# Kernel tuning notes

Hardware: AMD Instinct MI355X
Metric: run time of the kernel (lower is better)

## Reference

```python
import jax, jax.numpy as jnp
import numpy as np
from jax.scipy.linalg import solve_triangular

REG = 1e-6  # reg_covar added to covariance diagonal
LOG2PI = float(np.log(2.0 * np.pi))
RESP_EPS = 10.0 * float(np.finfo(np.float32).eps)


def _log_gauss(X, means, covs):
    # X: [N,D], means: [K,D], covs: [K,D,D] -> per-sample per-component log N(x|mu_k, Sigma_k): [N,K]
    K, D = means.shape
    eye = jnp.eye(D, dtype=X.dtype)
    chol = jnp.linalg.cholesky(covs + REG * eye)                      # [K,D,D]
    diff = X[None, :, :] - means[:, None, :]                          # [K,N,D]
    sol = jax.vmap(lambda L, d: solve_triangular(L, d.T, lower=True))(chol, diff)  # [K,D,N]
    maha = jnp.sum(sol * sol, axis=1)                                 # [K,N]
    logdet = jnp.sum(jnp.log(jnp.diagonal(chol, axis1=1, axis2=2)), axis=1)  # [K] = 0.5*log|Sigma|
    return (-0.5 * (D * LOG2PI + maha) - logdet[:, None]).T           # [N,K]


def _em_step(X, weights, means, covs):
    N, D = X.shape
    # E-step: responsibilities via stable logsumexp
    lp = _log_gauss(X, means, covs) + jnp.log(weights)[None, :]       # [N,K]
    log_norm = jax.scipy.special.logsumexp(lp, axis=1)                # [N]
    resp = jnp.exp(lp - log_norm[:, None])                            # [N,K]
    # M-step (MLE)
    nk = resp.sum(axis=0) + RESP_EPS                                  # [K]
    new_w = nk / N
    new_means = (resp.T @ X) / nk[:, None]                            # [K,D]
    diff = X[None, :, :] - new_means[:, None, :]                      # [K,N,D]
    new_covs = jnp.einsum('kn,knd,kne->kde', resp.T, diff, diff) / nk[:, None, None]
    new_covs = new_covs + REG * jnp.eye(D, dtype=X.dtype)
    return new_w, new_means, new_covs


def reference(X, weights, means, covariances, n_iter):
    # Normalize provided weights (uniform init in the torch module)
    w0 = weights / jnp.sum(weights)

    def step(carry, _):
        w, m, c = carry
        return _em_step(X, w, m, c), None

    (w, m, c), _ = jax.lax.scan(step, (w0, means, covariances), xs=None, length=n_iter)
    # Final per-sample log-likelihood under the fitted mixture (lower bound)
    lp = _log_gauss(X, m, c) + jnp.log(w)[None, :]
    return jax.scipy.special.logsumexp(lp, axis=1)                    # [N]


def setup_inputs() -> dict:
    key = jax.random.key(0)
    kx, km = jax.random.split(key)
    N, D, K = 100000, 32, 16
    X = jax.random.normal(kx, (N, D), dtype=jnp.float32)
    weights = jnp.ones((K,), dtype=jnp.float32) / K
    means = jax.random.normal(km, (K, D), dtype=jnp.float32)
    covariances = jnp.tile(jnp.eye(D, dtype=jnp.float32)[None], (K, 1, 1))
    return {"X": X, "weights": weights, "means": means, "covariances": covariances, "n_iter": 5}
```

## Files before the change

kernel.cpp:

```cpp
#include <hip/hip_runtime.h>
#include <math.h>

#define REGC 1e-6f
#define LOG2PI 1.83787706640934534f
#define RESP_EPS 1.1920929e-6f

#define PART_K 1156
#define RS 16

typedef __attribute__((ext_vector_type(8))) short short8;
typedef __attribute__((ext_vector_type(4))) float f32x4;
typedef unsigned short ushort_t;
typedef unsigned int uint_t;

__device__ __forceinline__ ushort_t f2bf(float x) {
    uint_t u = __float_as_uint(x);
    uint_t r = (u + 0x7fffu + ((u >> 16) & 1u)) >> 16;
    return (ushort_t)r;
}
__device__ __forceinline__ float bf2f(ushort_t h) {
    return __uint_as_float(((uint_t)h) << 16);
}
__device__ __forceinline__ f32x4 shx4(f32x4 v, int m) {
    f32x4 r;
#pragma unroll
    for (int i = 0; i < 4; ++i) r[i] = __shfl_xor(v[i], m);
    return r;
}
__device__ __forceinline__ f32x4 sel4(bool s, f32x4 b, f32x4 a) {
    f32x4 r;
#pragma unroll
    for (int i = 0; i < 4; ++i) r[i] = s ? b[i] : a[i];
    return r;
}
__device__ __forceinline__ short8 pack_rx(const float* r8, const short8 bh, float& row) {
    uint_t u[8];
#pragma unroll
    for (int jj = 0; jj < 8; ++jj) {
        float av = r8[jj] * bf2f((ushort_t)bh[jj]);
        row += av;
        u[jj] = __float_as_uint(av) + 0x8000u;
    }
    short8 out;
    uint_t* o = (uint_t*)&out;
    o[0] = __builtin_amdgcn_perm(u[1], u[0], 0x07060302);
    o[1] = __builtin_amdgcn_perm(u[3], u[2], 0x07060302);
    o[2] = __builtin_amdgcn_perm(u[5], u[4], 0x07060302);
    o[3] = __builtin_amdgcn_perm(u[7], u[6], 0x07060302);
    return out;
}

__global__ __launch_bounds__(256) void gmm_xsplit(const float* __restrict__ X,
                                                  ushort_t* __restrict__ Xh,
                                                  ushort_t* __restrict__ Xl,
                                                  ushort_t* __restrict__ XTH,
                                                  int N) {
    int chunk = blockIdx.x;
    int t = threadIdx.x;
    __shared__ float xsh[32][33];
    int s = t >> 3, q = t & 7;
    int n = chunk * 32 + s;
    float4 v = make_float4(0.f, 0.f, 0.f, 0.f);
    if (n < N) v = ((const float4*)(X + (size_t)n * 32))[q];
    float vv[4] = { v.x, v.y, v.z, v.w };
    xsh[s][q * 4 + 0] = v.x; xsh[s][q * 4 + 1] = v.y;
    xsh[s][q * 4 + 2] = v.z; xsh[s][q * 4 + 3] = v.w;
    if (n < N) {
        ushort_t h[4], l[4];
#pragma unroll
        for (int i = 0; i < 4; ++i) {
            h[i] = f2bf(vv[i]);
            l[i] = f2bf(vv[i] - bf2f(h[i]));
        }
        size_t o = (size_t)n * 32 + q * 4;
        *(uint2*)(Xh + o) = make_uint2((uint_t)h[0] | ((uint_t)h[1] << 16),
                                       (uint_t)h[2] | ((uint_t)h[3] << 16));
        *(uint2*)(Xl + o) = make_uint2((uint_t)l[0] | ((uint_t)l[1] << 16),
                                       (uint_t)l[2] | ((uint_t)l[3] << 16));
    }
    __syncthreads();
    int di = t >> 7;
    int lane = (t >> 1) & 63;
    int jj0 = (t & 1) * 4;
    int c = lane & 15, quad = lane >> 4;
    int d = di * 16 + c;
    ushort_t fh[4];
#pragma unroll
    for (int i = 0; i < 4; ++i) fh[i] = f2bf(xsh[quad * 8 + jj0 + i][d]);
    size_t fo = ((size_t)(chunk * 2 + di) * 64 + lane) * 8 + jj0;
    *(uint2*)(XTH + fo) = make_uint2((uint_t)fh[0] | ((uint_t)fh[1] << 16),
                                     (uint_t)fh[2] | ((uint_t)fh[3] << 16));
}

__global__ __launch_bounds__(64) void gmm_prep0(const float* __restrict__ w,
                                                const float* __restrict__ mu,
                                                const float* __restrict__ cov,
                                                ushort_t* __restrict__ Wh,
                                                ushort_t* __restrict__ Wl,
                                                float* __restrict__ Bv,
                                                float* __restrict__ Cc) {
    int k = blockIdx.x;
    int t = threadIdx.x;
    __shared__ float L[32][33];
    __shared__ float Ai[32][33];
    const float* cv = cov + (size_t)k * 1024;
    const float* muk = mu + (size_t)k * 32;
#pragma unroll
    for (int rep = 0; rep < 16; ++rep) {
        int idx = rep * 64 + t;
        int i = idx >> 5, j = idx & 31;
        L[i][j] = cv[idx] + (i == j ? REGC : 0.f);
    }
    __syncthreads();
#pragma unroll
    for (int j = 0; j < 32; ++j) {
        float s = L[j][j];
#pragma unroll
        for (int p = 0; p < j; ++p) { float v = L[j][p]; s -= v * v; }
        float dj = sqrtf(s);
        if (t > j && t < 32) {
            float s2 = L[t][j];
#pragma unroll
            for (int p = 0; p < j; ++p) s2 -= L[t][p] * L[j][p];
            L[t][j] = s2 / dj;
        }
        if (t == j) L[j][j] = dj;
        __syncthreads();
    }
    if (t < 32) {
        float ai[32];
#pragma unroll
        for (int r = 0; r < 32; ++r) {
            float s = (r == t) ? 1.f : 0.f;
#pragma unroll
            for (int p = 0; p < r; ++p) s -= L[r][p] * ai[p];
            ai[r] = s / L[r][r];
        }
#pragma unroll
        for (int r = 0; r < 32; ++r) Ai[r][t] = ai[r];
    }
    __syncthreads();
#pragma unroll
    for (int rep = 0; rep < 16; ++rep) {
        int idx = rep * 64 + t;
        int i = idx >> 5, j = idx & 31;
        float v = Ai[i][j];
        ushort_t h = f2bf(v);
        Wh[(size_t)(k * 32 + i) * 32 + j] = h;
        Wl[(size_t)(k * 32 + i) * 32 + j] = f2bf(v - bf2f(h));
    }
    if (t < 32) {
        float s = 0.f;
#pragma unroll
        for (int j = 0; j < 32; ++j) s += Ai[t][j] * muk[j];
        Bv[k * 32 + t] = s;
    }
    float wsum = 0.f;
#pragma unroll
    for (int i = 0; i < 16; ++i) wsum += w[i];
    float lv = (t < 32) ? logf(L[t & 31][t & 31]) : 0.f;
#pragma unroll
    for (int off = 1; off < 32; off <<= 1) lv += __shfl_xor(lv, off);
    if (t == 0) Cc[k] = logf(w[k] / wsum) - 0.5f * 32.0f * LOG2PI - lv;
}

__global__ __launch_bounds__(1024) __attribute__((amdgpu_waves_per_eu(4, 4)))
void gmm_emstep(const ushort_t* __restrict__ Xh, const ushort_t* __restrict__ Xl,
                const ushort_t* __restrict__ XTH,
                const ushort_t* __restrict__ Wh, const ushort_t* __restrict__ Wl,
                const float* __restrict__ Bv, const float* __restrict__ Cc,
                float* __restrict__ part, int N) {
    __shared__ float rsh[16][516];
    int t = threadIdx.x;
    int wave = t >> 6, lane = t & 63;
    int quad = lane >> 4, c = lane & 15;

    int wstart0 = (int)blockIdx.x * 512 + wave * 32;
    bool dup = (wstart0 + 32 > N);
    int wst = dup ? ((N >= 32) ? N - 32 : 0) : wstart0;

    size_t xo0 = (size_t)(wst + c) * 32 + quad * 8;
    size_t xo1 = (size_t)(wst + 16 + c) * 32 + quad * 8;
    short8 ah0 = *(const short8*)(Xh + xo0);
    short8 al0 = *(const short8*)(Xl + xo0);
    short8 ah1 = *(const short8*)(Xh + xo1);
    short8 al1 = *(const short8*)(Xl + xo1);

    {
        f32x4 p0[2], p1[2], p2[2], p3[2], fin[2];
#pragma unroll
        for (int k = 0; k < 16; ++k) {
            size_t w0 = (size_t)(k * 32 + c) * 32 + quad * 8;
            size_t w1 = w0 + 512;
            short8 bh0 = *(const short8*)(Wh + w0);
            short8 bl0 = *(const short8*)(Wl + w0);
            short8 bh1 = *(const short8*)(Wh + w1);
            short8 bl1 = *(const short8*)(Wl + w1);
            float bv0 = Bv[k * 32 + c];
            float bv1 = Bv[k * 32 + 16 + c];
#pragma unroll
            for (int tt = 0; tt < 2; ++tt) {
                short8 ah = tt ? ah1 : ah0;
                short8 al = tt ? al1 : al0;
                f32x4 a0 = {0.f, 0.f, 0.f, 0.f};
                f32x4 a1 = {0.f, 0.f, 0.f, 0.f};
                a0 = __builtin_amdgcn_mfma_f32_16x16x32_bf16(ah, bh0, a0, 0, 0, 0);
                a0 = __builtin_amdgcn_mfma_f32_16x16x32_bf16(ah, bl0, a0, 0, 0, 0);
                a0 = __builtin_amdgcn_mfma_f32_16x16x32_bf16(al, bh0, a0, 0, 0, 0);
                a1 = __builtin_amdgcn_mfma_f32_16x16x32_bf16(ah, bh1, a1, 0, 0, 0);
                a1 = __builtin_amdgcn_mfma_f32_16x16x32_bf16(ah, bl1, a1, 0, 0, 0);
                a1 = __builtin_amdgcn_mfma_f32_16x16x32_bf16(al, bh1, a1, 0, 0, 0);
                f32x4 ms;
#pragma unroll
                for (int r = 0; r < 4; ++r) {
                    float d0 = a0[r] - bv0;
                    float d1 = a1[r] - bv1;
                    ms[r] = fmaf(d0, d0, d1 * d1);
                }
                if ((k & 1) == 0) { p0[tt] = ms; }
                else {
                    f32x4 a = p0[tt] + shx4(p0[tt], 1);
                    f32x4 b = ms + shx4(ms, 1);
                    f32x4 v = sel4((c & 1) != 0, b, a);
                    if ((k & 2) == 0) { p1[tt] = v; }
                    else {
                        a = p1[tt] + shx4(p1[tt], 2); b = v + shx4(v, 2); v = sel4((c & 2) != 0, b, a);
                        if ((k & 4) == 0) { p2[tt] = v; }
                        else {
                            a = p2[tt] + shx4(p2[tt], 4); b = v + shx4(v, 4); v = sel4((c & 4) != 0, b, a);
                            if ((k & 8) == 0) { p3[tt] = v; }
                            else {
                                a = p3[tt] + shx4(p3[tt], 8); b = v + shx4(v, 8);
                                fin[tt] = sel4((c & 8) != 0, b, a);
                            }
                        }
                    }
                }
            }
        }
        float ccv = Cc[c];
#pragma unroll
        for (int tt = 0; tt < 2; ++tt) {
            f32x4 lp;
#pragma unroll
            for (int r = 0; r < 4; ++r) lp[r] = ccv - 0.5f * fin[tt][r];
            f32x4 mx = lp;
#pragma unroll
            for (int off = 1; off < 16; off <<= 1) {
                f32x4 s = shx4(mx, off);
#pragma unroll
                for (int r = 0; r < 4; ++r) mx[r] = fmaxf(mx[r], s[r]);
            }
            f32x4 e;
#pragma unroll
            for (int r = 0; r < 4; ++r) e[r] = __expf(lp[r] - mx[r]);
            f32x4 sm = e;
#pragma unroll
            for (int off = 1; off < 16; off <<= 1) sm = sm + shx4(sm, off);
            f32x4 sv;
#pragma unroll
            for (int r = 0; r < 4; ++r) sv[r] = dup ? 0.f : e[r] / sm[r];
            *(f32x4*)&rsh[c][wave * 32 + tt * 16 + quad * 4] = sv;
        }
    }
    __syncthreads();

    {
        int k = wave;
        f32x4 m00 = {0.f,0.f,0.f,0.f}, m01 = {0.f,0.f,0.f,0.f};
        f32x4 m10 = {0.f,0.f,0.f,0.f}, m11 = {0.f,0.f,0.f,0.f};
        float row0 = 0.f, row1 = 0.f, corner = 0.f;
#pragma unroll 4
        for (int ch = 0; ch < 16; ++ch) {
            size_t fb = (((size_t)((int)blockIdx.x * 16 + ch)) * 128 + lane) * 8;
            short8 bh0 = *(const short8*)(XTH + fb);
            short8 bh1 = *(const short8*)(XTH + fb + 512);
            float r8[8];
#pragma unroll
            for (int jj = 0; jj < 8; ++jj) r8[jj] = rsh[k][ch * 32 + quad * 8 + jj];
            corner += ((r8[0]+r8[1])+(r8[2]+r8[3])) + ((r8[4]+r8[5])+(r8[6]+r8[7]));
            short8 a0 = pack_rx(r8, bh0, row0);
            short8 a1 = pack_rx(r8, bh1, row1);
            m00 = __builtin_amdgcn_mfma_f32_16x16x32_bf16(a0, bh0, m00, 0, 0, 0);
            m01 = __builtin_amdgcn_mfma_f32_16x16x32_bf16(a0, bh1, m01, 0, 0, 0);
            m10 = __builtin_amdgcn_mfma_f32_16x16x32_bf16(a1, bh0, m10, 0, 0, 0);
            m11 = __builtin_amdgcn_mfma_f32_16x16x32_bf16(a1, bh1, m11, 0, 0, 0);
        }
        row0 += __shfl_xor(row0, 16);  row0 += __shfl_xor(row0, 32);
        row1 += __shfl_xor(row1, 16);  row1 += __shfl_xor(row1, 32);
        corner += __shfl_xor(corner, 16);  corner += __shfl_xor(corner, 32);

        float* pb = part + ((size_t)blockIdx.x * 16 + k) * PART_K;
#pragma unroll
        for (int r = 0; r < 4; ++r) {
            pb[(quad * 4 + r) * 34 + c]           = m00[r];
            pb[(quad * 4 + r) * 34 + 16 + c]      = m01[r];
            pb[(16 + quad * 4 + r) * 34 + c]      = m10[r];
            pb[(16 + quad * 4 + r) * 34 + 16 + c] = m11[r];
        }
        if (quad == 0) {
            pb[32 * 34 + c]      = row0;
            pb[32 * 34 + 16 + c] = row1;
        }
        if (lane == 0) pb[32 * 34 + 32] = corner;
    }
}

__global__ __launch_bounds__(256) void gmm_reduce1(const float* __restrict__ part,
                                                   float* __restrict__ part2,
                                                   int npart) {
    int k = blockIdx.x, g = blockIdx.y;
    int nb = (npart + RS - 1) / RS;
    int b0 = g * nb;
    int b1 = b0 + nb; if (b1 > npart) b1 = npart;
    for (int idx = threadIdx.x; idx < PART_K; idx += 256) {
        float s = 0.f;
#pragma unroll 4
        for (int b = b0; b < b1; ++b)
            s += part[((size_t)b * 16 + k) * PART_K + idx];
        part2[((size_t)g * 16 + k) * PART_K + idx] = s;
    }
}

__global__ __launch_bounds__(1024) void gmm_redfin_prep(const float* __restrict__ part2,
                                                        ushort_t* __restrict__ Wh,
                                                        ushort_t* __restrict__ Wl,
                                                        float* __restrict__ Bv,
                                                        float* __restrict__ Cc,
                                                        int N) {
    int k = blockIdx.x;
    int t = threadIdx.x;
    __shared__ float S[1156];
    __shared__ float L[1056];
    __shared__ float Ai[1056];
    __shared__ float mean[32];

    for (int idx = t; idx < 1121; idx += 1024) {
        float s = 0.f;
#pragma unroll
        for (int b = 0; b < RS; ++b)
            s += part2[((size_t)b * 16 + k) * PART_K + idx];
        S[idx] = s;
    }
    __syncthreads();
    float nk = S[32 * 34 + 32] + RESP_EPS;
    float inv = 1.f / nk;
    {
        int i = t >> 5, j = t & 31;
        float mi = S[32 * 34 + i] * inv;
        float mj = S[32 * 34 + j] * inv;
        L[i * 33 + j] = S[i * 34 + j] * inv - mi * mj + ((i == j) ? 2.f * REGC : 0.f);
    }
    if (t < 32) mean[t] = S[32 * 34 + t] * inv;
    __syncthreads();

#pragma unroll
    for (int j = 0; j < 32; ++j) {
        if (t < 32) {
            float s = L[j * 33 + j];
#pragma unroll
            for (int p = 0; p < j; ++p) { float v = L[j * 33 + p]; s -= v * v; }
            float dj = sqrtf(s);
            if (t > j) {
                float s2 = L[t * 33 + j];
#pragma unroll
                for (int p = 0; p < j; ++p) s2 -= L[t * 33 + p] * L[j * 33 + p];
                L[t * 33 + j] = s2 / dj;
            }
            if (t == j) L[j * 33 + j] = dj;
        }
        __syncthreads();
    }
    if (t < 32) {
        float ai[32];
#pragma unroll
        for (int r = 0; r < 32; ++r) {
            float s = (r == t) ? 1.f : 0.f;
#pragma unroll
            for (int p = 0; p < r; ++p) s -= L[r * 33 + p] * ai[p];
            ai[r] = s / L[r * 33 + r];
        }
#pragma unroll
        for (int r = 0; r < 32; ++r) Ai[r * 33 + t] = ai[r];
    }
    __syncthreads();
    {
        int i = t >> 5, j = t & 31;
        float v = Ai[i * 33 + j];
        ushort_t h = f2bf(v);
        Wh[(size_t)(k * 32 + i) * 32 + j] = h;
        Wl[(size_t)(k * 32 + i) * 32 + j] = f2bf(v - bf2f(h));
    }
    if (t < 32) {
        float s = 0.f;
#pragma unroll
        for (int j = 0; j < 32; ++j) s += Ai[t * 33 + j] * mean[j];
        Bv[k * 32 + t] = s;
    }
    float lv = (t < 32) ? logf(L[(t & 31) * 33 + (t & 31)]) : 0.f;
#pragma unroll
    for (int off = 1; off < 32; off <<= 1) lv += __shfl_xor(lv, off);
    if (t == 0) Cc[k] = logf(nk / (float)N) - 0.5f * 32.0f * LOG2PI - lv;
}

__global__ __launch_bounds__(256, 2) void gmm_estep_fin(const ushort_t* __restrict__ Xh,
                                                        const ushort_t* __restrict__ Xl,
                                                        const ushort_t* __restrict__ Wh,
                                                        const ushort_t* __restrict__ Wl,
                                                        const float* __restrict__ Bv,
                                                        const float* __restrict__ Cc,
                                                        float* __restrict__ out,
                                                        int N) {
    int t = threadIdx.x;
    int wave = t >> 6, lane = t & 63;
    int quad = lane >> 4, c = lane & 15;
    int wstart = (blockIdx.x * 4 + wave) * 32;
    if (wstart + 32 > N) wstart = (N >= 32) ? (N - 32) : 0;
    bool al4 = ((N & 3) == 0);

    size_t xo0 = (size_t)(wstart + c) * 32 + quad * 8;
    size_t xo1 = (size_t)(wstart + 16 + c) * 32 + quad * 8;
    short8 ah0 = *(const short8*)(Xh + xo0);
    short8 al0 = *(const short8*)(Xl + xo0);
    short8 ah1 = *(const short8*)(Xh + xo1);
    short8 al1 = *(const short8*)(Xl + xo1);

    f32x4 p0[2], p1[2], p2[2], p3[2], fin[2];
#pragma unroll
    for (int k = 0; k < 16; ++k) {
        size_t w0 = (size_t)(k * 32 + c) * 32 + quad * 8;
        size_t w1 = w0 + 512;
        short8 bh0 = *(const short8*)(Wh + w0);
        short8 bl0 = *(const short8*)(Wl + w0);
        short8 bh1 = *(const short8*)(Wh + w1);
        short8 bl1 = *(const short8*)(Wl + w1);
        float bv0 = Bv[k * 32 + c];
        float bv1 = Bv[k * 32 + 16 + c];
#pragma unroll
        for (int tt = 0; tt < 2; ++tt) {
            short8 ah = tt ? ah1 : ah0;
            short8 al = tt ? al1 : al0;
            f32x4 a0 = {0.f, 0.f, 0.f, 0.f};
            f32x4 a1 = {0.f, 0.f, 0.f, 0.f};
            a0 = __builtin_amdgcn_mfma_f32_16x16x32_bf16(ah, bh0, a0, 0, 0, 0);
            a0 = __builtin_amdgcn_mfma_f32_16x16x32_bf16(ah, bl0, a0, 0, 0, 0);
            a0 = __builtin_amdgcn_mfma_f32_16x16x32_bf16(al, bh0, a0, 0, 0, 0);
            a1 = __builtin_amdgcn_mfma_f32_16x16x32_bf16(ah, bh1, a1, 0, 0, 0);
            a1 = __builtin_amdgcn_mfma_f32_16x16x32_bf16(ah, bl1, a1, 0, 0, 0);
            a1 = __builtin_amdgcn_mfma_f32_16x16x32_bf16(al, bh1, a1, 0, 0, 0);
            f32x4 ms;
#pragma unroll
            for (int r = 0; r < 4; ++r) {
                float d0 = a0[r] - bv0;
                float d1 = a1[r] - bv1;
                ms[r] = fmaf(d0, d0, d1 * d1);
            }
            if ((k & 1) == 0) { p0[tt] = ms; }
            else {
                f32x4 a = p0[tt] + shx4(p0[tt], 1);
                f32x4 b = ms + shx4(ms, 1);
                f32x4 v = sel4((c & 1) != 0, b, a);
                if ((k & 2) == 0) { p1[tt] = v; }
                else {
                    a = p1[tt] + shx4(p1[tt], 2); b = v + shx4(v, 2); v = sel4((c & 2) != 0, b, a);
                    if ((k & 4) == 0) { p2[tt] = v; }
                    else {
                        a = p2[tt] + shx4(p2[tt], 4); b = v + shx4(v, 4); v = sel4((c & 4) != 0, b, a);
                        if ((k & 8) == 0) { p3[tt] = v; }
                        else {
                            a = p3[tt] + shx4(p3[tt], 8); b = v + shx4(v, 8);
                            fin[tt] = sel4((c & 8) != 0, b, a);
                        }
                    }
                }
            }
        }
    }
    float ccv = Cc[c];
#pragma unroll
    for (int tt = 0; tt < 2; ++tt) {
        f32x4 lp;
#pragma unroll
        for (int r = 0; r < 4; ++r) lp[r] = ccv - 0.5f * fin[tt][r];
        f32x4 mx = lp;
#pragma unroll
        for (int off = 1; off < 16; off <<= 1) {
            f32x4 s = shx4(mx, off);
#pragma unroll
            for (int r = 0; r < 4; ++r) mx[r] = fmaxf(mx[r], s[r]);
        }
        f32x4 e;
#pragma unroll
        for (int r = 0; r < 4; ++r) e[r] = __expf(lp[r] - mx[r]);
        f32x4 sm = e;
#pragma unroll
        for (int off = 1; off < 16; off <<= 1) sm = sm + shx4(sm, off);
        if (c == 0) {
            int nb = wstart + tt * 16 + quad * 4;
            f32x4 o;
#pragma unroll
            for (int r = 0; r < 4; ++r) o[r] = mx[r] + __logf(sm[r]);
            if (al4) *(f32x4*)(out + nb) = o;
            else { for (int r = 0; r < 4; ++r) out[nb + r] = o[r]; }
        }
    }
}

extern "C" void kernel_launch(void* const* d_in, const int* in_sizes, int n_in,
                              void* d_out, int out_size, void* d_ws, size_t ws_size,
                              hipStream_t stream) {
    const float* X   = (const float*)d_in[0];
    const float* w   = (const float*)d_in[1];
    const float* mu  = (const float*)d_in[2];
    const float* cov = (const float*)d_in[3];
    const int NITER = 5;
    int N = in_sizes[0] / 32;
    int NB = (N + 511) / 512;
    int NCB = NB * 16;

    float* ws = (float*)d_ws;
    float*    Bv = ws;
    float*    Cc = ws + 512;
    ushort_t* Wh = (ushort_t*)(ws + 528);
    ushort_t* Wl = (ushort_t*)(ws + 8720);
    ushort_t* Xh = (ushort_t*)(ws + 16912);
    ushort_t* Xl = (ushort_t*)(ws + 16912 + (size_t)16 * N);
    size_t xt0 = 16912 + (size_t)32 * N;
    size_t SZ  = (size_t)NCB * 512;
    ushort_t* XTH = (ushort_t*)(ws + xt0);
    float*  part2 = ws + xt0 + SZ;
    float*  part  = part2 + (size_t)RS * 16 * PART_K;

    float* out = (float*)d_out;

    int eblocks = ((N + 31) / 32 + 3) / 4;

    gmm_xsplit<<<NCB, 256, 0, stream>>>(X, Xh, Xl, XTH, N);
    gmm_prep0<<<16, 64, 0, stream>>>(w, mu, cov, Wh, Wl, Bv, Cc);

    for (int it = 0; it < NITER; ++it) {
        gmm_emstep<<<NB, 1024, 0, stream>>>(Xh, Xl, XTH, Wh, Wl, Bv, Cc, part, N);
        dim3 r1(16, RS);
        gmm_reduce1<<<r1, 256, 0, stream>>>(part, part2, NB);
        gmm_redfin_prep<<<16, 1024, 0, stream>>>(part2, Wh, Wl, Bv, Cc, N);
    }
    gmm_estep_fin<<<eblocks, 256, 0, stream>>>(Xh, Xl, Wh, Wl, Bv, Cc, out, N);
}
```

Before: 454.8 us.

## Split fused EM step into E-step and moment kernels with symmetric partials

The fused per-block E/M kernel is split in two. One kernel computes responsibilities with the whitening matrices staged in LDS and writes them to a global buffer. A second kernel accumulates the moment matrices for two components per wave using MFMA. Only the upper triangle of each symmetric second-moment matrix is computed and stored, which cuts MFMAs and partial-sum traffic, and the finalize kernel rebuilds the full covariance from the packed form. The cost is an extra launch per iteration and a global round trip for the responsibility array.

```diff
diff --git a/kernel.cpp b/kernel.cpp
--- a/kernel.cpp
+++ b/kernel.cpp
@@ -5,7 +5,7 @@
 #define LOG2PI 1.83787706640934534f
 #define RESP_EPS 1.1920929e-6f
 
-#define PART_K 1156
+#define PART_K 561
 #define RS 16
 
 typedef __attribute__((ext_vector_type(8))) short short8;
@@ -164,145 +164,177 @@
     if (t == 0) Cc[k] = logf(w[k] / wsum) - 0.5f * 32.0f * LOG2PI - lv;
 }
 
-__global__ __launch_bounds__(1024) __attribute__((amdgpu_waves_per_eu(4, 4)))
-void gmm_emstep(const ushort_t* __restrict__ Xh, const ushort_t* __restrict__ Xl,
-                const ushort_t* __restrict__ XTH,
-                const ushort_t* __restrict__ Wh, const ushort_t* __restrict__ Wl,
-                const float* __restrict__ Bv, const float* __restrict__ Cc,
-                float* __restrict__ part, int N) {
-    __shared__ float rsh[16][516];
+__global__ __launch_bounds__(1024) __attribute__((amdgpu_waves_per_eu(8)))
+void gmm_estep(const ushort_t* __restrict__ Xh, const ushort_t* __restrict__ Xl,
+               const ushort_t* __restrict__ Wh, const ushort_t* __restrict__ Wl,
+               const float* __restrict__ Bv, const float* __restrict__ Cc,
+               float* __restrict__ resp, int N, int Ns) {
+    __shared__ ushort_t WhL[16384];
+    __shared__ ushort_t WlL[16384];
+    __shared__ float BvL[512];
+    __shared__ float CcL[16];
+    int t = threadIdx.x;
+    {
+        const uint4* srcH = (const uint4*)Wh;
+        const uint4* srcL = (const uint4*)Wl;
+        uint4* dstH = (uint4*)WhL;
+        uint4* dstL = (uint4*)WlL;
+#pragma unroll 2
+        for (int i = t; i < 2048; i += 1024) { dstH[i] = srcH[i]; dstL[i] = srcL[i]; }
+        if (t < 512) BvL[t] = Bv[t];
+        if (t < 16) CcL[t] = Cc[t];
+    }
+    __syncthreads();
+
+    int wave = t >> 6, lane = t & 63;
+    int quad = lane >> 4, c = lane & 15;
+    int w0 = (int)blockIdx.x * 256 + wave * 16;
+    if (w0 + 16 > N) w0 = (N >= 16) ? (N - 16) : 0;
+
+    size_t xo = (size_t)(w0 + c) * 32 + quad * 8;
+    short8 ah = *(const short8*)(Xh + xo);
+    short8 al = *(const short8*)(Xl + xo);
+
+    f32x4 p0, p1, p2, p3, fin;
+#pragma unroll
+    for (int k = 0; k < 16; ++k) {
+        int wi = (k * 32 + c) * 32 + quad * 8;
+        short8 bh0 = *(const short8*)(WhL + wi);
+        short8 bl0 = *(const short8*)(WlL + wi);
+        short8 bh1 = *(const short8*)(WhL + wi + 512);
+        short8 bl1 = *(const short8*)(WlL + wi + 512);
+        float bv0 = BvL[k * 32 + c];
+        float bv1 = BvL[k * 32 + 16 + c];
+        f32x4 a0 = {0.f, 0.f, 0.f, 0.f};
+        f32x4 a1 = {0.f, 0.f, 0.f, 0.f};
+        a0 = __builtin_amdgcn_mfma_f32_16x16x32_bf16(ah, bh0, a0, 0, 0, 0);
+        a0 = __builtin_amdgcn_mfma_f32_16x16x32_bf16(ah, bl0, a0, 0, 0, 0);
+        a0 = __builtin_amdgcn_mfma_f32_16x16x32_bf16(al, bh0, a0, 0, 0, 0);
+        a1 = __builtin_amdgcn_mfma_f32_16x16x32_bf16(ah, bh1, a1, 0, 0, 0);
+        a1 = __builtin_amdgcn_mfma_f32_16x16x32_bf16(ah, bl1, a1, 0, 0, 0);
+        a1 = __builtin_amdgcn_mfma_f32_16x16x32_bf16(al, bh1, a1, 0, 0, 0);
+        f32x4 ms;
+#pragma unroll
+        for (int r = 0; r < 4; ++r) {
+            float d0 = a0[r] - bv0;
+            float d1 = a1[r] - bv1;
+            ms[r] = fmaf(d0, d0, d1 * d1);
+        }
+        if ((k & 1) == 0) { p0 = ms; }
+        else {
+            f32x4 a = p0 + shx4(p0, 1);
+            f32x4 b = ms + shx4(ms, 1);
+            f32x4 v = sel4((c & 1) != 0, b, a);
+            if ((k & 2) == 0) { p1 = v; }
+            else {
+                a = p1 + shx4(p1, 2); b = v + shx4(v, 2); v = sel4((c & 2) != 0, b, a);
+                if ((k & 4) == 0) { p2 = v; }
+                else {
+                    a = p2 + shx4(p2, 4); b = v + shx4(v, 4); v = sel4((c & 4) != 0, b, a);
+                    if ((k & 8) == 0) { p3 = v; }
+                    else {
+                        a = p3 + shx4(p3, 8); b = v + shx4(v, 8);
+                        fin = sel4((c & 8) != 0, b, a);
+                    }
+                }
+            }
+        }
+    }
+    float ccv = CcL[c];
+    f32x4 lp;
+#pragma unroll
+    for (int r = 0; r < 4; ++r) lp[r] = ccv - 0.5f * fin[r];
+    f32x4 mx = lp;
+#pragma unroll
+    for (int off = 1; off < 16; off <<= 1) {
+        f32x4 s = shx4(mx, off);
+#pragma unroll
+        for (int r = 0; r < 4; ++r) mx[r] = fmaxf(mx[r], s[r]);
+    }
+    f32x4 e;
+#pragma unroll
+    for (int r = 0; r < 4; ++r) e[r] = __expf(lp[r] - mx[r]);
+    f32x4 sm = e;
+#pragma unroll
+    for (int off = 1; off < 16; off <<= 1) sm = sm + shx4(sm, off);
+    f32x4 sv;
+#pragma unroll
+    for (int r = 0; r < 4; ++r) sv[r] = e[r] / sm[r];
+    float* rp = resp + (size_t)c * Ns + w0 + quad * 4;
+    if ((w0 & 3) == 0) *(f32x4*)rp = sv;
+    else { for (int r = 0; r < 4; ++r) rp[r] = sv[r]; }
+
+    int tail = Ns - N;
+    if (blockIdx.x == 0 && tail > 0) {
+        for (int i = t; i < 16 * tail; i += 1024) {
+            int kk = i / tail, n = i - kk * tail;
+            resp[(size_t)kk * Ns + N + n] = 0.f;
+        }
+    }
+}
+
+__global__ __launch_bounds__(512) __attribute__((amdgpu_waves_per_eu(4)))
+void gmm_moment(const ushort_t* __restrict__ XTH, const float* __restrict__ resp,
+                float* __restrict__ part, int Ns) {
     int t = threadIdx.x;
     int wave = t >> 6, lane = t & 63;
     int quad = lane >> 4, c = lane & 15;
 
-    int wstart0 = (int)blockIdx.x * 512 + wave * 32;
-    bool dup = (wstart0 + 32 > N);
-    int wst = dup ? ((N >= 32) ? N - 32 : 0) : wstart0;
-
-    size_t xo0 = (size_t)(wst + c) * 32 + quad * 8;
-    size_t xo1 = (size_t)(wst + 16 + c) * 32 + quad * 8;
-    short8 ah0 = *(const short8*)(Xh + xo0);
-    short8 al0 = *(const short8*)(Xl + xo0);
-    short8 ah1 = *(const short8*)(Xh + xo1);
-    short8 al1 = *(const short8*)(Xl + xo1);
-
-    {
-        f32x4 p0[2], p1[2], p2[2], p3[2], fin[2];
-#pragma unroll
-        for (int k = 0; k < 16; ++k) {
-            size_t w0 = (size_t)(k * 32 + c) * 32 + quad * 8;
-            size_t w1 = w0 + 512;
-            short8 bh0 = *(const short8*)(Wh + w0);
-            short8 bl0 = *(const short8*)(Wl + w0);
-            short8 bh1 = *(const short8*)(Wh + w1);
-            short8 bl1 = *(const short8*)(Wl + w1);
-            float bv0 = Bv[k * 32 + c];
-            float bv1 = Bv[k * 32 + 16 + c];
-#pragma unroll
-            for (int tt = 0; tt < 2; ++tt) {
-                short8 ah = tt ? ah1 : ah0;
-                short8 al = tt ? al1 : al0;
-                f32x4 a0 = {0.f, 0.f, 0.f, 0.f};
-                f32x4 a1 = {0.f, 0.f, 0.f, 0.f};
-                a0 = __builtin_amdgcn_mfma_f32_16x16x32_bf16(ah, bh0, a0, 0, 0, 0);
-                a0 = __builtin_amdgcn_mfma_f32_16x16x32_bf16(ah, bl0, a0, 0, 0, 0);
-                a0 = __builtin_amdgcn_mfma_f32_16x16x32_bf16(al, bh0, a0, 0, 0, 0);
-                a1 = __builtin_amdgcn_mfma_f32_16x16x32_bf16(ah, bh1, a1, 0, 0, 0);
-                a1 = __builtin_amdgcn_mfma_f32_16x16x32_bf16(ah, bl1, a1, 0, 0, 0);
-                a1 = __builtin_amdgcn_mfma_f32_16x16x32_bf16(al, bh1, a1, 0, 0, 0);
-                f32x4 ms;
-#pragma unroll
-                for (int r = 0; r < 4; ++r) {
-                    float d0 = a0[r] - bv0;
-                    float d1 = a1[r] - bv1;
-                    ms[r] = fmaf(d0, d0, d1 * d1);
-                }
-                if ((k & 1) == 0) { p0[tt] = ms; }
-                else {
-                    f32x4 a = p0[tt] + shx4(p0[tt], 1);
-                    f32x4 b = ms + shx4(ms, 1);
-                    f32x4 v = sel4((c & 1) != 0, b, a);
-                    if ((k & 2) == 0) { p1[tt] = v; }
-                    else {
-                        a = p1[tt] + shx4(p1[tt], 2); b = v + shx4(v, 2); v = sel4((c & 2) != 0, b, a);
-                        if ((k & 4) == 0) { p2[tt] = v; }
-                        else {
-                            a = p2[tt] + shx4(p2[tt], 4); b = v + shx4(v, 4); v = sel4((c & 4) != 0, b, a);
-                            if ((k & 8) == 0) { p3[tt] = v; }
-                            else {
-                                a = p3[tt] + shx4(p3[tt], 8); b = v + shx4(v, 8);
-                                fin[tt] = sel4((c & 8) != 0, b, a);
-                            }
-                        }
-                    }
-                }
-            }
-        }
-        float ccv = Cc[c];
-#pragma unroll
-        for (int tt = 0; tt < 2; ++tt) {
-            f32x4 lp;
-#pragma unroll
-            for (int r = 0; r < 4; ++r) lp[r] = ccv - 0.5f * fin[tt][r];
-            f32x4 mx = lp;
-#pragma unroll
-            for (int off = 1; off < 16; off <<= 1) {
-                f32x4 s = shx4(mx, off);
-#pragma unroll
-                for (int r = 0; r < 4; ++r) mx[r] = fmaxf(mx[r], s[r]);
-            }
-            f32x4 e;
-#pragma unroll
-            for (int r = 0; r < 4; ++r) e[r] = __expf(lp[r] - mx[r]);
-            f32x4 sm = e;
-#pragma unroll
-            for (int off = 1; off < 16; off <<= 1) sm = sm + shx4(sm, off);
-            f32x4 sv;
-#pragma unroll
-            for (int r = 0; r < 4; ++r) sv[r] = dup ? 0.f : e[r] / sm[r];
-            *(f32x4*)&rsh[c][wave * 32 + tt * 16 + quad * 4] = sv;
-        }
-    }
-    __syncthreads();
-
-    {
-        int k = wave;
-        f32x4 m00 = {0.f,0.f,0.f,0.f}, m01 = {0.f,0.f,0.f,0.f};
-        f32x4 m10 = {0.f,0.f,0.f,0.f}, m11 = {0.f,0.f,0.f,0.f};
-        float row0 = 0.f, row1 = 0.f, corner = 0.f;
-#pragma unroll 4
-        for (int ch = 0; ch < 16; ++ch) {
-            size_t fb = (((size_t)((int)blockIdx.x * 16 + ch)) * 128 + lane) * 8;
-            short8 bh0 = *(const short8*)(XTH + fb);
-            short8 bh1 = *(const short8*)(XTH + fb + 512);
-            float r8[8];
-#pragma unroll
-            for (int jj = 0; jj < 8; ++jj) r8[jj] = rsh[k][ch * 32 + quad * 8 + jj];
-            corner += ((r8[0]+r8[1])+(r8[2]+r8[3])) + ((r8[4]+r8[5])+(r8[6]+r8[7]));
-            short8 a0 = pack_rx(r8, bh0, row0);
-            short8 a1 = pack_rx(r8, bh1, row1);
-            m00 = __builtin_amdgcn_mfma_f32_16x16x32_bf16(a0, bh0, m00, 0, 0, 0);
-            m01 = __builtin_amdgcn_mfma_f32_16x16x32_bf16(a0, bh1, m01, 0, 0, 0);
-            m10 = __builtin_amdgcn_mfma_f32_16x16x32_bf16(a1, bh0, m10, 0, 0, 0);
-            m11 = __builtin_amdgcn_mfma_f32_16x16x32_bf16(a1, bh1, m11, 0, 0, 0);
-        }
-        row0 += __shfl_xor(row0, 16);  row0 += __shfl_xor(row0, 32);
-        row1 += __shfl_xor(row1, 16);  row1 += __shfl_xor(row1, 32);
-        corner += __shfl_xor(corner, 16);  corner += __shfl_xor(corner, 32);
-
+    f32x4 q00[2], q01[2], q11[2];
+#pragma unroll
+    for (int kk = 0; kk < 2; ++kk) {
+        q00[kk] = (f32x4){0.f, 0.f, 0.f, 0.f};
+        q01[kk] = (f32x4){0.f, 0.f, 0.f, 0.f};
+        q11[kk] = (f32x4){0.f, 0.f, 0.f, 0.f};
+    }
+    float row0[2] = {0.f, 0.f}, row1[2] = {0.f, 0.f}, corner[2] = {0.f, 0.f};
+
+#pragma unroll 2
+    for (int ch = 0; ch < 8; ++ch) {
+        int gch = (int)blockIdx.x * 8 + ch;
+        size_t fb = ((size_t)gch * 128 + lane) * 8;
+        short8 bh0 = *(const short8*)(XTH + fb);
+        short8 bh1 = *(const short8*)(XTH + fb + 512);
+        int n0 = gch * 32 + quad * 8;
+#pragma unroll
+        for (int kk = 0; kk < 2; ++kk) {
+            int k = wave + kk * 8;
+            const float* rp = resp + (size_t)k * Ns + n0;
+            f32x4 rv0 = *(const f32x4*)rp;
+            f32x4 rv1 = *(const f32x4*)(rp + 4);
+            float r8[8] = { rv0[0], rv0[1], rv0[2], rv0[3],
+                            rv1[0], rv1[1], rv1[2], rv1[3] };
+            corner[kk] += ((r8[0] + r8[1]) + (r8[2] + r8[3])) +
+                          ((r8[4] + r8[5]) + (r8[6] + r8[7]));
+            short8 a0 = pack_rx(r8, bh0, row0[kk]);
+            short8 a1 = pack_rx(r8, bh1, row1[kk]);
+            q00[kk] = __builtin_amdgcn_mfma_f32_16x16x32_bf16(a0, bh0, q00[kk], 0, 0, 0);
+            q01[kk] = __builtin_amdgcn_mfma_f32_16x16x32_bf16(a0, bh1, q01[kk], 0, 0, 0);
+            q11[kk] = __builtin_amdgcn_mfma_f32_16x16x32_bf16(a1, bh1, q11[kk], 0, 0, 0);
+        }
+    }
+#pragma unroll
+    for (int kk = 0; kk < 2; ++kk) {
+        row0[kk] += __shfl_xor(row0[kk], 16);  row0[kk] += __shfl_xor(row0[kk], 32);
+        row1[kk] += __shfl_xor(row1[kk], 16);  row1[kk] += __shfl_xor(row1[kk], 32);
+        corner[kk] += __shfl_xor(corner[kk], 16);  corner[kk] += __shfl_xor(corner[kk], 32);
+
+        int k = wave + kk * 8;
         float* pb = part + ((size_t)blockIdx.x * 16 + k) * PART_K;
 #pragma unroll
         for (int r = 0; r < 4; ++r) {
-            pb[(quad * 4 + r) * 34 + c]           = m00[r];
-            pb[(quad * 4 + r) * 34 + 16 + c]      = m01[r];
-            pb[(16 + quad * 4 + r) * 34 + c]      = m10[r];
-            pb[(16 + quad * 4 + r) * 34 + 16 + c] = m11[r];
+            int i = quad * 4 + r;
+            int base = i * 32 - ((i * (i + 1)) >> 1);
+            if (c >= i) pb[base + c] = q00[kk][r];
+            pb[base + 16 + c] = q01[kk][r];
+            int i2 = 16 + i;
+            if (c >= i) pb[i2 * 32 - ((i2 * (i2 + 1)) >> 1) + 16 + c] = q11[kk][r];
         }
         if (quad == 0) {
-            pb[32 * 34 + c]      = row0;
-            pb[32 * 34 + 16 + c] = row1;
-        }
-        if (lane == 0) pb[32 * 34 + 32] = corner;
+            pb[528 + c] = row0[kk];
+            pb[528 + 16 + c] = row1[kk];
+        }
+        if (lane == 0) pb[560] = corner[kk];
     }
 }
 
@@ -322,20 +354,20 @@
     }
 }
 
-__global__ __launch_bounds__(1024) void gmm_redfin_prep(const float* __restrict__ part2,
-                                                        ushort_t* __restrict__ Wh,
-                                                        ushort_t* __restrict__ Wl,
-                                                        float* __restrict__ Bv,
-                                                        float* __restrict__ Cc,
-                                                        int N) {
+__global__ __launch_bounds__(256) void gmm_redfin_prep(const float* __restrict__ part2,
+                                                       ushort_t* __restrict__ Wh,
+                                                       ushort_t* __restrict__ Wl,
+                                                       float* __restrict__ Bv,
+                                                       float* __restrict__ Cc,
+                                                       int N) {
     int k = blockIdx.x;
     int t = threadIdx.x;
-    __shared__ float S[1156];
+    __shared__ float S[561];
     __shared__ float L[1056];
     __shared__ float Ai[1056];
     __shared__ float mean[32];
 
-    for (int idx = t; idx < 1121; idx += 1024) {
+    for (int idx = t; idx < PART_K; idx += 256) {
         float s = 0.f;
 #pragma unroll
         for (int b = 0; b < RS; ++b)
@@ -343,15 +375,18 @@
         S[idx] = s;
     }
     __syncthreads();
-    float nk = S[32 * 34 + 32] + RESP_EPS;
+    float nk = S[560] + RESP_EPS;
     float inv = 1.f / nk;
-    {
-        int i = t >> 5, j = t & 31;
-        float mi = S[32 * 34 + i] * inv;
-        float mj = S[32 * 34 + j] * inv;
-        L[i * 33 + j] = S[i * 34 + j] * inv - mi * mj + ((i == j) ? 2.f * REGC : 0.f);
-    }
-    if (t < 32) mean[t] = S[32 * 34 + t] * inv;
+    if (t < 32) mean[t] = S[528 + t] * inv;
+    __syncthreads();
+#pragma unroll
+    for (int i0 = 0; i0 < 4; ++i0) {
+        int i = i0 * 8 + (t >> 5), j = t & 31;
+        int a = i < j ? i : j;
+        int b2 = i < j ? j : i;
+        float cv = S[a * 32 - ((a * (a + 1)) >> 1) + b2];
+        L[i * 33 + j] = cv * inv - mean[i] * mean[j] + ((i == j) ? 2.f * REGC : 0.f);
+    }
     __syncthreads();
 
 #pragma unroll
@@ -384,8 +419,9 @@
         for (int r = 0; r < 32; ++r) Ai[r * 33 + t] = ai[r];
     }
     __syncthreads();
-    {
-        int i = t >> 5, j = t & 31;
+#pragma unroll
+    for (int i0 = 0; i0 < 4; ++i0) {
+        int i = i0 * 8 + (t >> 5), j = t & 31;
         float v = Ai[i * 33 + j];
         ushort_t h = f2bf(v);
         Wh[(size_t)(k * 32 + i) * 32 + j] = h;
@@ -515,8 +551,9 @@
     const float* cov = (const float*)d_in[3];
     const int NITER = 5;
     int N = in_sizes[0] / 32;
-    int NB = (N + 511) / 512;
-    int NCB = NB * 16;
+    int MB = (N + 255) / 256;
+    int NCB = MB * 8;
+    int Ns = MB * 256;
 
     float* ws = (float*)d_ws;
     float*    Bv = ws;
@@ -526,9 +563,10 @@
     ushort_t* Xh = (ushort_t*)(ws + 16912);
     ushort_t* Xl = (ushort_t*)(ws + 16912 + (size_t)16 * N);
     size_t xt0 = 16912 + (size_t)32 * N;
-    size_t SZ  = (size_t)NCB * 512;
+    size_t XTHf = (size_t)NCB * 512;
     ushort_t* XTH = (ushort_t*)(ws + xt0);
-    float*  part2 = ws + xt0 + SZ;
+    float*  resp  = ws + xt0 + XTHf;
+    float*  part2 = resp + (size_t)16 * Ns;
     float*  part  = part2 + (size_t)RS * 16 * PART_K;
 
     float* out = (float*)d_out;
@@ -539,10 +577,11 @@
     gmm_prep0<<<16, 64, 0, stream>>>(w, mu, cov, Wh, Wl, Bv, Cc);
 
     for (int it = 0; it < NITER; ++it) {
-        gmm_emstep<<<NB, 1024, 0, stream>>>(Xh, Xl, XTH, Wh, Wl, Bv, Cc, part, N);
+        gmm_estep<<<MB, 1024, 0, stream>>>(Xh, Xl, Wh, Wl, Bv, Cc, resp, N, Ns);
+        gmm_moment<<<MB, 512, 0, stream>>>(XTH, resp, part, Ns);
         dim3 r1(16, RS);
-        gmm_reduce1<<<r1, 256, 0, stream>>>(part, part2, NB);
-        gmm_redfin_prep<<<16, 1024, 0, stream>>>(part2, Wh, Wl, Bv, Cc, N);
+        gmm_reduce1<<<r1, 256, 0, stream>>>(part, part2, MB);
+        gmm_redfin_prep<<<16, 256, 0, stream>>>(part2, Wh, Wl, Bv, Cc, N);
     }
     gmm_estep_fin<<<eblocks, 256, 0, stream>>>(Xh, Xl, Wh, Wl, Bv, Cc, out, N);
 }
```

After: 486.9 us. +7.1%, slower.

## Exploit covariance symmetry and halve emstep block size with two components per wave

Applied to the files above, without the earlier changes.

The M-step scatter matrix is symmetric, so only the upper triangle is accumulated and stored. This drops one of the four MFMAs per chunk and packs the partials into 561 floats per component instead of 1156. The emstep block shrinks to 512 threads over 256 rows, with each wave handling two components, and waves_per_eu is relaxed to allow more residency. The final reduce kernel now unpacks the triangular layout with 256 threads. The cost is some extra index arithmetic and more blocks, so the total partial traffic changes little.

```diff
diff --git a/kernel.cpp b/kernel.cpp
--- a/kernel.cpp
+++ b/kernel.cpp
@@ -5,7 +5,7 @@
 #define LOG2PI 1.83787706640934534f
 #define RESP_EPS 1.1920929e-6f
 
-#define PART_K 1156
+#define PART_K 561
 #define RS 16
 
 typedef __attribute__((ext_vector_type(8))) short short8;
@@ -164,18 +164,18 @@
     if (t == 0) Cc[k] = logf(w[k] / wsum) - 0.5f * 32.0f * LOG2PI - lv;
 }
 
-__global__ __launch_bounds__(1024) __attribute__((amdgpu_waves_per_eu(4, 4)))
+__global__ __launch_bounds__(512) __attribute__((amdgpu_waves_per_eu(6)))
 void gmm_emstep(const ushort_t* __restrict__ Xh, const ushort_t* __restrict__ Xl,
                 const ushort_t* __restrict__ XTH,
                 const ushort_t* __restrict__ Wh, const ushort_t* __restrict__ Wl,
                 const float* __restrict__ Bv, const float* __restrict__ Cc,
                 float* __restrict__ part, int N) {
-    __shared__ float rsh[16][516];
+    __shared__ float rsh[16][260];
     int t = threadIdx.x;
     int wave = t >> 6, lane = t & 63;
     int quad = lane >> 4, c = lane & 15;
 
-    int wstart0 = (int)blockIdx.x * 512 + wave * 32;
+    int wstart0 = (int)blockIdx.x * 256 + wave * 32;
     bool dup = (wstart0 + 32 > N);
     int wst = dup ? ((N >= 32) ? N - 32 : 0) : wstart0;
 
@@ -266,43 +266,58 @@
     __syncthreads();
 
     {
-        int k = wave;
-        f32x4 m00 = {0.f,0.f,0.f,0.f}, m01 = {0.f,0.f,0.f,0.f};
-        f32x4 m10 = {0.f,0.f,0.f,0.f}, m11 = {0.f,0.f,0.f,0.f};
-        float row0 = 0.f, row1 = 0.f, corner = 0.f;
-#pragma unroll 4
-        for (int ch = 0; ch < 16; ++ch) {
-            size_t fb = (((size_t)((int)blockIdx.x * 16 + ch)) * 128 + lane) * 8;
+        f32x4 q00[2], q01[2], q11[2];
+#pragma unroll
+        for (int kk = 0; kk < 2; ++kk) {
+            q00[kk] = (f32x4){0.f, 0.f, 0.f, 0.f};
+            q01[kk] = (f32x4){0.f, 0.f, 0.f, 0.f};
+            q11[kk] = (f32x4){0.f, 0.f, 0.f, 0.f};
+        }
+        float row0[2] = {0.f, 0.f}, row1[2] = {0.f, 0.f}, corner[2] = {0.f, 0.f};
+
+#pragma unroll 2
+        for (int ch = 0; ch < 8; ++ch) {
+            size_t fb = (((size_t)((int)blockIdx.x * 8 + ch)) * 128 + lane) * 8;
             short8 bh0 = *(const short8*)(XTH + fb);
             short8 bh1 = *(const short8*)(XTH + fb + 512);
-            float r8[8];
-#pragma unroll
-            for (int jj = 0; jj < 8; ++jj) r8[jj] = rsh[k][ch * 32 + quad * 8 + jj];
-            corner += ((r8[0]+r8[1])+(r8[2]+r8[3])) + ((r8[4]+r8[5])+(r8[6]+r8[7]));
-            short8 a0 = pack_rx(r8, bh0, row0);
-            short8 a1 = pack_rx(r8, bh1, row1);
-            m00 = __builtin_amdgcn_mfma_f32_16x16x32_bf16(a0, bh0, m00, 0, 0, 0);
-            m01 = __builtin_amdgcn_mfma_f32_16x16x32_bf16(a0, bh1, m01, 0, 0, 0);
-            m10 = __builtin_amdgcn_mfma_f32_16x16x32_bf16(a1, bh0, m10, 0, 0, 0);
-            m11 = __builtin_amdgcn_mfma_f32_16x16x32_bf16(a1, bh1, m11, 0, 0, 0);
-        }
-        row0 += __shfl_xor(row0, 16);  row0 += __shfl_xor(row0, 32);
-        row1 += __shfl_xor(row1, 16);  row1 += __shfl_xor(row1, 32);
-        corner += __shfl_xor(corner, 16);  corner += __shfl_xor(corner, 32);
-
-        float* pb = part + ((size_t)blockIdx.x * 16 + k) * PART_K;
-#pragma unroll
-        for (int r = 0; r < 4; ++r) {
-            pb[(quad * 4 + r) * 34 + c]           = m00[r];
-            pb[(quad * 4 + r) * 34 + 16 + c]      = m01[r];
-            pb[(16 + quad * 4 + r) * 34 + c]      = m10[r];
-            pb[(16 + quad * 4 + r) * 34 + 16 + c] = m11[r];
-        }
-        if (quad == 0) {
-            pb[32 * 34 + c]      = row0;
-            pb[32 * 34 + 16 + c] = row1;
-        }
-        if (lane == 0) pb[32 * 34 + 32] = corner;
+#pragma unroll
+            for (int kk = 0; kk < 2; ++kk) {
+                int k = wave + kk * 8;
+                float r8[8];
+#pragma unroll
+                for (int jj = 0; jj < 8; ++jj) r8[jj] = rsh[k][ch * 32 + quad * 8 + jj];
+                corner[kk] += ((r8[0] + r8[1]) + (r8[2] + r8[3])) +
+                              ((r8[4] + r8[5]) + (r8[6] + r8[7]));
+                short8 a0 = pack_rx(r8, bh0, row0[kk]);
+                short8 a1 = pack_rx(r8, bh1, row1[kk]);
+                q00[kk] = __builtin_amdgcn_mfma_f32_16x16x32_bf16(a0, bh0, q00[kk], 0, 0, 0);
+                q01[kk] = __builtin_amdgcn_mfma_f32_16x16x32_bf16(a0, bh1, q01[kk], 0, 0, 0);
+                q11[kk] = __builtin_amdgcn_mfma_f32_16x16x32_bf16(a1, bh1, q11[kk], 0, 0, 0);
+            }
+        }
+#pragma unroll
+        for (int kk = 0; kk < 2; ++kk) {
+            row0[kk] += __shfl_xor(row0[kk], 16);  row0[kk] += __shfl_xor(row0[kk], 32);
+            row1[kk] += __shfl_xor(row1[kk], 16);  row1[kk] += __shfl_xor(row1[kk], 32);
+            corner[kk] += __shfl_xor(corner[kk], 16);  corner[kk] += __shfl_xor(corner[kk], 32);
+
+            int k = wave + kk * 8;
+            float* pb = part + ((size_t)blockIdx.x * 16 + k) * PART_K;
+#pragma unroll
+            for (int r = 0; r < 4; ++r) {
+                int i = quad * 4 + r;
+                int base = i * 32 - ((i * (i + 1)) >> 1);
+                if (c >= i) pb[base + c] = q00[kk][r];
+                pb[base + 16 + c] = q01[kk][r];
+                int i2 = 16 + i;
+                if (c >= i) pb[i2 * 32 - ((i2 * (i2 + 1)) >> 1) + 16 + c] = q11[kk][r];
+            }
+            if (quad == 0) {
+                pb[528 + c] = row0[kk];
+                pb[528 + 16 + c] = row1[kk];
+            }
+            if (lane == 0) pb[560] = corner[kk];
+        }
     }
 }
 
@@ -322,20 +337,20 @@
     }
 }
 
-__global__ __launch_bounds__(1024) void gmm_redfin_prep(const float* __restrict__ part2,
-                                                        ushort_t* __restrict__ Wh,
-                                                        ushort_t* __restrict__ Wl,
-                                                        float* __restrict__ Bv,
-                                                        float* __restrict__ Cc,
-                                                        int N) {
+__global__ __launch_bounds__(256) void gmm_redfin_prep(const float* __restrict__ part2,
+                                                       ushort_t* __restrict__ Wh,
+                                                       ushort_t* __restrict__ Wl,
+                                                       float* __restrict__ Bv,
+                                                       float* __restrict__ Cc,
+                                                       int N) {
     int k = blockIdx.x;
     int t = threadIdx.x;
-    __shared__ float S[1156];
+    __shared__ float S[561];
     __shared__ float L[1056];
     __shared__ float Ai[1056];
     __shared__ float mean[32];
 
-    for (int idx = t; idx < 1121; idx += 1024) {
+    for (int idx = t; idx < PART_K; idx += 256) {
         float s = 0.f;
 #pragma unroll
         for (int b = 0; b < RS; ++b)
@@ -343,15 +358,18 @@
         S[idx] = s;
     }
     __syncthreads();
-    float nk = S[32 * 34 + 32] + RESP_EPS;
+    float nk = S[560] + RESP_EPS;
     float inv = 1.f / nk;
-    {
-        int i = t >> 5, j = t & 31;
-        float mi = S[32 * 34 + i] * inv;
-        float mj = S[32 * 34 + j] * inv;
-        L[i * 33 + j] = S[i * 34 + j] * inv - mi * mj + ((i == j) ? 2.f * REGC : 0.f);
-    }
-    if (t < 32) mean[t] = S[32 * 34 + t] * inv;
+    if (t < 32) mean[t] = S[528 + t] * inv;
+    __syncthreads();
+#pragma unroll
+    for (int i0 = 0; i0 < 4; ++i0) {
+        int i = i0 * 8 + (t >> 5), j = t & 31;
+        int a = i < j ? i : j;
+        int b2 = i < j ? j : i;
+        float cv = S[a * 32 - ((a * (a + 1)) >> 1) + b2];
+        L[i * 33 + j] = cv * inv - mean[i] * mean[j] + ((i == j) ? 2.f * REGC : 0.f);
+    }
     __syncthreads();
 
 #pragma unroll
@@ -384,8 +402,9 @@
         for (int r = 0; r < 32; ++r) Ai[r * 33 + t] = ai[r];
     }
     __syncthreads();
-    {
-        int i = t >> 5, j = t & 31;
+#pragma unroll
+    for (int i0 = 0; i0 < 4; ++i0) {
+        int i = i0 * 8 + (t >> 5), j = t & 31;
         float v = Ai[i * 33 + j];
         ushort_t h = f2bf(v);
         Wh[(size_t)(k * 32 + i) * 32 + j] = h;
@@ -515,8 +534,8 @@
     const float* cov = (const float*)d_in[3];
     const int NITER = 5;
     int N = in_sizes[0] / 32;
-    int NB = (N + 511) / 512;
-    int NCB = NB * 16;
+    int MB = (N + 255) / 256;
+    int NCB = MB * 8;
 
     float* ws = (float*)d_ws;
     float*    Bv = ws;
@@ -526,9 +545,9 @@
     ushort_t* Xh = (ushort_t*)(ws + 16912);
     ushort_t* Xl = (ushort_t*)(ws + 16912 + (size_t)16 * N);
     size_t xt0 = 16912 + (size_t)32 * N;
-    size_t SZ  = (size_t)NCB * 512;
+    size_t XTHf = (size_t)NCB * 512;
     ushort_t* XTH = (ushort_t*)(ws + xt0);
-    float*  part2 = ws + xt0 + SZ;
+    float*  part2 = ws + xt0 + XTHf;
     float*  part  = part2 + (size_t)RS * 16 * PART_K;
 
     float* out = (float*)d_out;
@@ -539,10 +558,10 @@
     gmm_prep0<<<16, 64, 0, stream>>>(w, mu, cov, Wh, Wl, Bv, Cc);
 
     for (int it = 0; it < NITER; ++it) {
-        gmm_emstep<<<NB, 1024, 0, stream>>>(Xh, Xl, XTH, Wh, Wl, Bv, Cc, part, N);
+        gmm_emstep<<<MB, 512, 0, stream>>>(Xh, Xl, XTH, Wh, Wl, Bv, Cc, part, N);
         dim3 r1(16, RS);
-        gmm_reduce1<<<r1, 256, 0, stream>>>(part, part2, NB);
-        gmm_redfin_prep<<<16, 1024, 0, stream>>>(part2, Wh, Wl, Bv, Cc, N);
+        gmm_reduce1<<<r1, 256, 0, stream>>>(part, part2, MB);
+        gmm_redfin_prep<<<16, 256, 0, stream>>>(part2, Wh, Wl, Bv, Cc, N);
     }
     gmm_estep_fin<<<eblocks, 256, 0, stream>>>(Xh, Xl, Wh, Wl, Bv, Cc, out, N);
 }
```

Result: slower. 621.3 us (+36.6%).
